# Kernel tuning notes

Hardware: AMD Instinct MI355X
Metric: run time of the kernel (lower is better)

Reference implementation:

```python
import jax, jax.numpy as jnp
import numpy as np

D_MODEL = 1024
NUM_HEADS = 16
HEAD_DIM = D_MODEL // NUM_HEADS


def setup_inputs() -> dict:
    key = jax.random.key(0)
    ks = jax.random.split(key, 11)
    S, B, D = 2048, 2, D_MODEL
    scale = 1.0 / np.sqrt(D)
    inp = {
        'query': jax.random.normal(ks[0], (S, B, D), dtype=jnp.float32),
        'key': jax.random.normal(ks[1], (S, B, D), dtype=jnp.float32),
        'value': jax.random.normal(ks[2], (S, B, D), dtype=jnp.float32),
        'Wq': jax.random.normal(ks[3], (D, D), dtype=jnp.float32) * scale,
        'bq': jnp.zeros((D,), dtype=jnp.float32),
        'Wk': jax.random.normal(ks[4], (D, D), dtype=jnp.float32) * scale,
        'bk': jnp.zeros((D,), dtype=jnp.float32),
        'Wv': jax.random.normal(ks[5], (D, D), dtype=jnp.float32) * scale,
        'bv': jnp.zeros((D,), dtype=jnp.float32),
        'Wo': jax.random.normal(ks[6], (D, D), dtype=jnp.float32) * scale,
        'bo': jnp.zeros((D,), dtype=jnp.float32),
    }
    return inp


def reference(query, key, value, Wq, bq, Wk, bk, Wv, bv, Wo, bo):
    # query/key/value: [S, B, D] (seq-first, as in the torch module)
    S, B, D = query.shape
    H, Hd = NUM_HEADS, HEAD_DIM
    # Linear: x @ W.T + b (torch convention), then split heads -> [B, H, S, Hd]
    def proj_heads(x, W, b):
        y = jnp.einsum('sbd,ed->sbe', x, W) + b  # [S, B, D]
        return y.reshape(x.shape[0], B, H, Hd).transpose(1, 2, 0, 3)
    q = proj_heads(query, Wq, bq)   # [B, H, S, Hd]
    k = proj_heads(key, Wk, bk)     # [B, H, Sk, Hd]
    v = proj_heads(value, Wv, bv)   # [B, H, Sk, Hd]
    scores = jnp.einsum('bhsd,bhtd->bhst', q, k) / jnp.sqrt(jnp.asarray(Hd, q.dtype))
    probs = jax.nn.softmax(scores, axis=-1)  # dropout p=0.0 -> identity
    attn = jnp.einsum('bhst,bhtd->bhsd', probs, v)  # [B, H, S, Hd]
    attn = attn.transpose(2, 0, 1, 3).reshape(S, B, D)  # [S, B, D]
    out = jnp.einsum('sbd,ed->sbe', attn, Wo) + bo
    return out
```

## Files before the change

kernel.cpp:

```cpp
#include <hip/hip_runtime.h>
#include <stdint.h>

#define S_LEN 2048
#define BATCH 2
#define DM    1024
#define NH    16
#define HD    64
#define MROWS 4096

typedef float f32x4 __attribute__((ext_vector_type(4)));
typedef short bfrag __attribute__((ext_vector_type(8)));
typedef unsigned short u16x4_t __attribute__((ext_vector_type(4)));
typedef unsigned short u16x8_t __attribute__((ext_vector_type(8)));
typedef int i32x4_t __attribute__((ext_vector_type(4)));

#define EXP2F(x) __builtin_amdgcn_exp2f(x)

__device__ inline f32x4 mfma16(bfrag a, bfrag b, f32x4 c) {
    return __builtin_amdgcn_mfma_f32_16x16x32_bf16(a, b, c, 0, 0, 0);
}

__device__ inline unsigned short bf16_rn(float x) {
    unsigned u = __builtin_bit_cast(unsigned, x);
    return (unsigned short)((u + 0x7fffu + ((u >> 16) & 1u)) >> 16);
}

__device__ inline void split_bf16(float x, unsigned short &h, unsigned short &l) {
    unsigned u = __builtin_bit_cast(unsigned, x);
    h = (unsigned short)(u >> 16);
    float hf = __builtin_bit_cast(float, u & 0xffff0000u);
    float r = x - hf;
    l = (unsigned short)(__builtin_bit_cast(unsigned, r) >> 16);
}

__device__ inline unsigned pack_rhu(float a, float b) {
    unsigned ua = __builtin_bit_cast(unsigned, a) + 0x8000u;
    unsigned ub = __builtin_bit_cast(unsigned, b) + 0x8000u;
    return (ua >> 16) | (ub & 0xffff0000u);
}

typedef __attribute__((address_space(1))) const unsigned int as1_u32;
typedef __attribute__((address_space(3))) unsigned int as3_u32;
__device__ inline void async16(void* lds, const void* g) {
    __builtin_amdgcn_global_load_lds((as1_u32*)g, (as3_u32*)lds, 16, 0, 0);
}

__global__ __launch_bounds__(256)
void cvt_kernel(const float* __restrict__ Wq, const float* __restrict__ Wk,
                const float* __restrict__ Wv, const float* __restrict__ Wo,
                const float* __restrict__ Qin, const float* __restrict__ Kin,
                const float* __restrict__ Vin,
                unsigned short* __restrict__ Wqb, unsigned short* __restrict__ Wkb,
                unsigned short* __restrict__ Wvb,
                unsigned short* __restrict__ Woh, unsigned short* __restrict__ Wol,
                unsigned short* __restrict__ Qa,  unsigned short* __restrict__ Ka,
                unsigned short* __restrict__ Va)
{
    const int z = blockIdx.z;
    size_t idx = ((size_t)blockIdx.x * 256 + threadIdx.x) * 8;
    const size_t limit = (z < 4) ? (size_t)DM * DM : (size_t)MROWS * DM;
    if (idx >= limit) return;
    const float* src = (z == 0) ? Wq : (z == 1) ? Wk : (z == 2) ? Wv :
                       (z == 3) ? Wo : (z == 4) ? Qin : (z == 5) ? Kin : Vin;
    float4 f0 = *(const float4*)&src[idx];
    float4 f1 = *(const float4*)&src[idx + 4];
    if (z != 3) {
        unsigned short* dst = (z == 0) ? Wqb : (z == 1) ? Wkb : (z == 2) ? Wvb :
                              (z == 4) ? Qa  : (z == 5) ? Ka  : Va;
        u16x8_t v = { bf16_rn(f0.x), bf16_rn(f0.y), bf16_rn(f0.z), bf16_rn(f0.w),
                      bf16_rn(f1.x), bf16_rn(f1.y), bf16_rn(f1.z), bf16_rn(f1.w) };
        *(u16x8_t*)&dst[idx] = v;
    } else {
        unsigned short h0,h1,h2,h3,h4,h5,h6,h7, l0,l1,l2,l3,l4,l5,l6,l7;
        split_bf16(f0.x,h0,l0); split_bf16(f0.y,h1,l1);
        split_bf16(f0.z,h2,l2); split_bf16(f0.w,h3,l3);
        split_bf16(f1.x,h4,l4); split_bf16(f1.y,h5,l5);
        split_bf16(f1.z,h6,l6); split_bf16(f1.w,h7,l7);
        u16x8_t vh = {h0,h1,h2,h3,h4,h5,h6,h7};
        u16x8_t vl = {l0,l1,l2,l3,l4,l5,l6,l7};
        *(u16x8_t*)&Woh[idx] = vh;
        *(u16x8_t*)&Wol[idx] = vl;
    }
}

__global__ __launch_bounds__(256)
void qkv_gemm(const unsigned short* __restrict__ Qa,
              const unsigned short* __restrict__ Ka,
              const unsigned short* __restrict__ Va,
              const unsigned short* __restrict__ Wqb,
              const unsigned short* __restrict__ Wkb,
              const unsigned short* __restrict__ Wvb,
              const float* __restrict__ bq, const float* __restrict__ bk,
              const float* __restrict__ bv,
              unsigned short* __restrict__ Qb, unsigned short* __restrict__ Kb,
              unsigned short* __restrict__ Vt)
{
    __shared__ unsigned short sA[128*32];
    __shared__ unsigned short sB[128*32];

    const int tid = threadIdx.x, lane = tid & 63, w4 = tid >> 6;
    const int m16 = lane & 15, q4 = lane >> 4;
    const int wr = w4 >> 1, wc = w4 & 1;
    const int z = blockIdx.z;

    int id = blockIdx.x + 8 * blockIdx.y;
    int j  = id >> 3;
    const int m0 = ((id & 7) * 4 + (j & 3)) * 128;
    const int n0 = (j >> 2) * 128;

    const unsigned short* A = (z == 0) ? Qa : (z == 1) ? Ka : Va;
    const unsigned short* W = (z == 0) ? Wqb : (z == 1) ? Wkb : Wvb;
    const float* bias = (z == 0) ? bq : (z == 1) ? bk : bv;
    unsigned short* outp = (z == 0) ? Qb : (z == 1) ? Kb : Vt;

    const int G1 = tid + 256;
    const int r0 = tid >> 2, g0 = (tid & 3) ^ ((r0 ^ (r0 >> 2)) & 3);
    const int r1 = G1  >> 2, g1 = (G1  & 3) ^ ((r1 ^ (r1 >> 2)) & 3);
    const char* gA0 = (const char*)A + (size_t)(m0 + r0) * 2048 + g0 * 16;
    const char* gA1 = (const char*)A + (size_t)(m0 + r1) * 2048 + g1 * 16;
    const char* gB0 = (const char*)W + (size_t)(n0 + r0) * 2048 + g0 * 16;
    const char* gB1 = (const char*)W + (size_t)(n0 + r1) * 2048 + g1 * 16;
    char* ldsA0 = (char*)sA + w4 * 1024;
    char* ldsA1 = (char*)sA + 4096 + w4 * 1024;
    char* ldsB0 = (char*)sB + w4 * 1024;
    char* ldsB1 = (char*)sB + 4096 + w4 * 1024;

    int offA[4], offB[4];
    #pragma unroll
    for (int rt = 0; rt < 4; rt++) {
        int r = wr * 64 + rt * 16 + m16;
        offA[rt] = r * 32 + ((q4 ^ ((r ^ (r >> 2)) & 3)) << 3);
    }
    #pragma unroll
    for (int ct = 0; ct < 4; ct++) {
        int r = wc * 64 + ct * 16 + m16;
        offB[ct] = r * 32 + ((q4 ^ ((r ^ (r >> 2)) & 3)) << 3);
    }

    f32x4 acc[4][4];
    const f32x4 zero4 = {0.f, 0.f, 0.f, 0.f};
    #pragma unroll
    for (int i = 0; i < 4; i++)
        #pragma unroll
        for (int jj = 0; jj < 4; jj++) acc[i][jj] = zero4;

    for (int k0 = 0; k0 < DM; k0 += 32) {
        async16(ldsA0, gA0);
        async16(ldsA1, gA1);
        async16(ldsB0, gB0);
        async16(ldsB1, gB1);
        gA0 += 64; gA1 += 64; gB0 += 64; gB1 += 64;
        __syncthreads();

        bfrag a[4], bb[4];
        #pragma unroll
        for (int rt = 0; rt < 4; rt++) a[rt]  = *(const bfrag*)&sA[offA[rt]];
        #pragma unroll
        for (int ct = 0; ct < 4; ct++) bb[ct] = *(const bfrag*)&sB[offB[ct]];

        #pragma unroll
        for (int rt = 0; rt < 4; rt++)
            #pragma unroll
            for (int ct = 0; ct < 4; ct++)
                acc[rt][ct] = mfma16(a[rt], bb[ct], acc[rt][ct]);
        __syncthreads();
    }

    const float SCALE = (z == 0) ? 0.18033688011112042f : 1.0f;
    #pragma unroll
    for (int rt = 0; rt < 4; rt++)
        #pragma unroll
        for (int ct = 0; ct < 4; ct++)
            #pragma unroll
            for (int reg = 0; reg < 4; reg++) {
                int r = m0 + wr * 64 + rt * 16 + q4 * 4 + reg;
                int c = n0 + wc * 64 + ct * 16 + m16;
                float v = (acc[rt][ct][reg] + bias[c]) * SCALE;
                int s = r >> 1, b = r & 1, hh = c >> 6, d = c & 63;
                unsigned short bv16 = bf16_rn(v);
                if (z == 2)
                    outp[((size_t)(b * NH + hh) * HD + d) * S_LEN + s] = bv16;
                else
                    outp[((size_t)(b * NH + hh) * S_LEN + s) * HD + d] = bv16;
            }
}

__global__ __launch_bounds__(256)
void attn_kernel(const unsigned short* __restrict__ Qb,
                 const unsigned short* __restrict__ Kb,
                 const unsigned short* __restrict__ Vt,
                 unsigned short* __restrict__ Ap)
{
    __shared__ unsigned short sK[2][64*64];
    __shared__ unsigned short sV[2][64*64];
    __shared__ unsigned int   sPT[4][32*36];

    const int tid = threadIdx.x, lane = tid & 63, w4 = tid >> 6;
    const int m16 = lane & 15, q4 = lane >> 4;

    int id = blockIdx.x;
    int xcd = id & 7, jj = id >> 3;
    const int bh = xcd * 4 + (jj >> 4);
    const int qc = jj & 15;
    const int b = bh >> 4, h = bh & 15;
    const int qw = qc * 128 + w4 * 32;

    const unsigned short* Qp = Qb + (size_t)bh * (S_LEN * HD);
    const unsigned short* Kp = Kb + (size_t)bh * (S_LEN * HD);
    const unsigned short* Vp = Vt + (size_t)bh * (S_LEN * HD);
    unsigned int* pw = sPT[w4];

    bfrag aq[2][2];
    #pragma unroll
    for (int nt = 0; nt < 2; nt++)
        #pragma unroll
        for (int kc = 0; kc < 2; kc++)
            aq[nt][kc] = *(const bfrag*)&Qp[(size_t)(qw + nt*16 + m16) * HD + kc*32 + q4*8];

    const int r0 = tid >> 3,         g0 = (tid & 7) ^ (r0 & 7);
    const int r1 = (tid + 256) >> 3, g1 = (tid & 7) ^ (r1 & 7);
    const char* gK0 = (const char*)Kp + (size_t)r0 * 128  + g0 * 16;
    const char* gK1 = (const char*)Kp + (size_t)r1 * 128  + g1 * 16;
    const char* gV0 = (const char*)Vp + (size_t)r0 * 4096 + g0 * 16;
    const char* gV1 = (const char*)Vp + (size_t)r1 * 4096 + g1 * 16;
    const int ldsw = w4 * 1024;

    const f32x4 zero4 = {0.f, 0.f, 0.f, 0.f};
    f32x4 O[2][4];
    float lp[2] = {0.f, 0.f};
    #pragma unroll
    for (int nt = 0; nt < 2; nt++)
        #pragma unroll
        for (int dt = 0; dt < 4; dt++) O[nt][dt] = zero4;

    async16((char*)sK[0] + ldsw,        gK0);
    async16((char*)sK[0] + 4096 + ldsw, gK1);
    async16((char*)sV[0] + ldsw,        gV0);
    async16((char*)sV[0] + 4096 + ldsw, gV1);

    const int NT = S_LEN / 64;
    for (int it = 0; it < NT; it++) {
        const int bi = it & 1;
        __syncthreads();
        if (it + 1 < NT) {
            size_t ko = (size_t)(it + 1) * 8192, vo = (size_t)(it + 1) * 128;
            async16((char*)sK[bi^1] + ldsw,        gK0 + ko);
            async16((char*)sK[bi^1] + 4096 + ldsw, gK1 + ko);
            async16((char*)sV[bi^1] + ldsw,        gV0 + vo);
            async16((char*)sV[bi^1] + 4096 + ldsw, gV1 + vo);
        }

        const unsigned short* kb = sK[bi];
        const unsigned short* vb = sV[bi];

        bfrag ak[4][2];
        #pragma unroll
        for (int mt = 0; mt < 4; mt++) {
            int r = mt*16 + m16, s = r & 7;
            ak[mt][0] = *(const bfrag*)&kb[r*64 + ((q4     ^ s) << 3)];
            ak[mt][1] = *(const bfrag*)&kb[r*64 + (((4+q4) ^ s) << 3)];
        }

        #pragma unroll
        for (int nt = 0; nt < 2; nt++) {
            f32x4 Sc[4];
            #pragma unroll
            for (int mt = 0; mt < 4; mt++) {
                Sc[mt] = mfma16(ak[mt][0], aq[nt][0], zero4);
                Sc[mt] = mfma16(ak[mt][1], aq[nt][1], Sc[mt]);
            }
            unsigned rowb = (unsigned)(nt*16 + m16) * 36;
            #pragma unroll
            for (int mt = 0; mt < 4; mt++) {
                float p0 = EXP2F(Sc[mt][0]), p1 = EXP2F(Sc[mt][1]);
                float p2 = EXP2F(Sc[mt][2]), p3 = EXP2F(Sc[mt][3]);
                unsigned c0 = pack_rhu(p0, p1);
                unsigned c1 = pack_rhu(p2, p3);
                float u0 = __builtin_bit_cast(float, c0 << 16);
                float u1 = __builtin_bit_cast(float, c0 & 0xffff0000u);
                float u2 = __builtin_bit_cast(float, c1 << 16);
                float u3 = __builtin_bit_cast(float, c1 & 0xffff0000u);
                lp[nt] += (u0 + u1) + (u2 + u3);
                uint2 c2 = { c0, c1 };
                *(uint2*)&pw[rowb + mt*8 + q4*2] = c2;
            }
        }

        bfrag av[4][2];
        #pragma unroll
        for (int dt = 0; dt < 4; dt++) {
            int r = dt*16 + m16, s = r & 7;
            av[dt][0] = *(const bfrag*)&vb[r*64 + ((q4     ^ s) << 3)];
            av[dt][1] = *(const bfrag*)&vb[r*64 + (((4+q4) ^ s) << 3)];
        }

        #pragma unroll
        for (int nt = 0; nt < 2; nt++) {
            bfrag bp[2];
            #pragma unroll
            for (int kc = 0; kc < 2; kc++)
                bp[kc] = __builtin_bit_cast(bfrag,
                    *(const i32x4_t*)&pw[(unsigned)(nt*16 + m16) * 36 + kc*16 + q4*4]);
            #pragma unroll
            for (int dt = 0; dt < 4; dt++) {
                O[nt][dt] = mfma16(av[dt][0], bp[0], O[nt][dt]);
                O[nt][dt] = mfma16(av[dt][1], bp[1], O[nt][dt]);
            }
        }
    }

    #pragma unroll
    for (int nt = 0; nt < 2; nt++) {
        float l = lp[nt];
        l += __shfl_xor(l, 16);
        l += __shfl_xor(l, 32);
        float inv = 1.0f / l;
        int q = qw + nt*16 + m16;
        size_t rb = ((size_t)q * BATCH + b) * DM + h * 64;
        #pragma unroll
        for (int dt = 0; dt < 4; dt++) {
            u16x4_t o = { bf16_rn(O[nt][dt][0] * inv), bf16_rn(O[nt][dt][1] * inv),
                          bf16_rn(O[nt][dt][2] * inv), bf16_rn(O[nt][dt][3] * inv) };
            *(u16x4_t*)&Ap[rb + dt*16 + q4*4] = o;
        }
    }
}

__global__ __launch_bounds__(512)
void out_gemm(const unsigned short* __restrict__ Ap,
              const unsigned short* __restrict__ Woh,
              const unsigned short* __restrict__ Wol,
              const float* __restrict__ bo, float* __restrict__ out)
{
    __shared__ unsigned short sA[128*32];
    __shared__ unsigned short sH[128*32];
    __shared__ unsigned short sL[128*32];

    const int tid = threadIdx.x, lane = tid & 63, w8 = tid >> 6;
    const int m16 = lane & 15, q4 = lane >> 4;
    const int wr = w8 >> 2, wc = w8 & 3;

    int id = blockIdx.x + 8 * blockIdx.y;
    int j  = id >> 3;
    const int m0 = ((id & 7) * 4 + (j & 3)) * 128;
    const int n0 = (j >> 2) * 128;

    const int br = tid >> 2,  bc = (tid & 3) ^ ((br ^ (br >> 2)) & 3);
    const unsigned short* gA = Ap  + (size_t)(m0 + br) * DM + bc * 8;
    const unsigned short* gH = Woh + (size_t)(n0 + br) * DM + bc * 8;
    const unsigned short* gL = Wol + (size_t)(n0 + br) * DM + bc * 8;
    unsigned short* ldsA = &sA[w8 * 512];
    unsigned short* ldsH = &sH[w8 * 512];
    unsigned short* ldsL = &sL[w8 * 512];

    int offA[4], offB[2];
    #pragma unroll
    for (int rt = 0; rt < 4; rt++) {
        int r = wr * 64 + rt * 16 + m16;
        offA[rt] = r * 32 + ((q4 ^ ((r ^ (r >> 2)) & 3)) << 3);
    }
    #pragma unroll
    for (int ct = 0; ct < 2; ct++) {
        int r = wc * 32 + ct * 16 + m16;
        offB[ct] = r * 32 + ((q4 ^ ((r ^ (r >> 2)) & 3)) << 3);
    }

    f32x4 acc[4][2];
    const f32x4 zero4 = {0.f, 0.f, 0.f, 0.f};
    #pragma unroll
    for (int i = 0; i < 4; i++)
        #pragma unroll
        for (int jj = 0; jj < 2; jj++) acc[i][jj] = zero4;

    for (int k0 = 0; k0 < DM; k0 += 32) {
        async16(ldsA, gA);
        async16(ldsH, gH);
        async16(ldsL, gL);
        gA += 32; gH += 32; gL += 32;
        __syncthreads();

        bfrag a[4], bh2[2], bl2[2];
        #pragma unroll
        for (int rt = 0; rt < 4; rt++) a[rt] = *(const bfrag*)&sA[offA[rt]];
        #pragma unroll
        for (int ct = 0; ct < 2; ct++) {
            bh2[ct] = *(const bfrag*)&sH[offB[ct]];
            bl2[ct] = *(const bfrag*)&sL[offB[ct]];
        }
        #pragma unroll
        for (int rt = 0; rt < 4; rt++)
            #pragma unroll
            for (int ct = 0; ct < 2; ct++) {
                acc[rt][ct] = mfma16(a[rt], bh2[ct], acc[rt][ct]);
                acc[rt][ct] = mfma16(a[rt], bl2[ct], acc[rt][ct]);
            }
        __syncthreads();
    }

    #pragma unroll
    for (int rt = 0; rt < 4; rt++)
        #pragma unroll
        for (int ct = 0; ct < 2; ct++)
            #pragma unroll
            for (int reg = 0; reg < 4; reg++) {
                int r = m0 + wr * 64 + rt * 16 + q4 * 4 + reg;
                int c = n0 + wc * 32 + ct * 16 + m16;
                out[(size_t)r * DM + c] = acc[rt][ct][reg] + bo[c];
            }
}

extern "C" void kernel_launch(void* const* d_in, const int* in_sizes, int n_in,
                              void* d_out, int out_size, void* d_ws, size_t ws_size,
                              hipStream_t stream)
{
    const float* query = (const float*)d_in[0];
    const float* key   = (const float*)d_in[1];
    const float* value = (const float*)d_in[2];
    const float* Wq    = (const float*)d_in[3];
    const float* bq    = (const float*)d_in[4];
    const float* Wk    = (const float*)d_in[5];
    const float* bk    = (const float*)d_in[6];
    const float* Wv    = (const float*)d_in[7];
    const float* bv    = (const float*)d_in[8];
    const float* Wo    = (const float*)d_in[9];
    const float* bo    = (const float*)d_in[10];

    char* ws = (char*)d_ws;
    const size_t MB = 1u << 20;
    unsigned short* Qb  = (unsigned short*)(ws);
    unsigned short* Kb  = (unsigned short*)(ws +  8*MB);
    unsigned short* Vt  = (unsigned short*)(ws + 16*MB);
    unsigned short* Woh = (unsigned short*)(ws + 24*MB);
    unsigned short* Wol = (unsigned short*)(ws + 26*MB);
    unsigned short* Wqb = (unsigned short*)(ws + 28*MB);
    unsigned short* Wkb = (unsigned short*)(ws + 30*MB);
    unsigned short* Wvb = (unsigned short*)(ws + 32*MB);
    unsigned short* Va  = (unsigned short*)(ws + 34*MB);
    unsigned short* Ap  = (unsigned short*)(ws + 28*MB);
    unsigned short* Qa  = (unsigned short*)d_out;
    unsigned short* Ka  = (unsigned short*)d_out + (size_t)MROWS*DM;

    cvt_kernel<<<dim3(2048, 1, 7), 256, 0, stream>>>(
        Wq, Wk, Wv, Wo, query, key, value,
        Wqb, Wkb, Wvb, Woh, Wol, Qa, Ka, Va);
    qkv_gemm<<<dim3(8, 32, 3), 256, 0, stream>>>(
        Qa, Ka, Va, Wqb, Wkb, Wvb, bq, bk, bv, Qb, Kb, Vt);
    attn_kernel<<<dim3(512), 256, 0, stream>>>(Qb, Kb, Vt, Ap);
    out_gemm<<<dim3(8, 32), 512, 0, stream>>>(Ap, Woh, Wol, bo, (float*)d_out);
}
```

Baseline: 243.8 us.

## Split attention over key halves with combine kernel and retile output GEMM

The attention kernel now splits the key/value sequence into two halves, doubling the grid to 1024 blocks. Each block writes unnormalized bf16 partial outputs and row sums, and a new combine kernel adds the halves, normalizes, and writes the head-interleaved layout. The output GEMM is retiled to 256 threads with 128x64 tiles and twice as many blocks. This aims to improve CU occupancy and load balance, at the cost of an extra kernel launch, extra memory traffic for the partials, and an extra bf16 rounding of the partial outputs. The row sum also now accumulates unrounded probabilities.

```diff
diff --git a/kernel.cpp b/kernel.cpp
--- a/kernel.cpp
+++ b/kernel.cpp
@@ -189,7 +189,8 @@
 void attn_kernel(const unsigned short* __restrict__ Qb,
                  const unsigned short* __restrict__ Kb,
                  const unsigned short* __restrict__ Vt,
-                 unsigned short* __restrict__ Ap)
+                 unsigned short* __restrict__ Op,
+                 float* __restrict__ Lp)
 {
     __shared__ unsigned short sK[2][64*64];
     __shared__ unsigned short sV[2][64*64];
@@ -199,11 +200,13 @@
     const int m16 = lane & 15, q4 = lane >> 4;
 
     int id = blockIdx.x;
-    int xcd = id & 7, jj = id >> 3;
-    const int bh = xcd * 4 + (jj >> 4);
-    const int qc = jj & 15;
-    const int b = bh >> 4, h = bh & 15;
-    const int qw = qc * 128 + w4 * 32;
+    int xcd = id & 7, j = id >> 3;
+    const int bh   = xcd * 4 + (j >> 5);
+    const int rem  = j & 31;
+    const int half = rem & 1;
+    const int qc   = rem >> 1;
+    const int qw   = qc * 128 + w4 * 32;
+    const int tbase = half * (S_LEN / 2);
 
     const unsigned short* Qp = Qb + (size_t)bh * (S_LEN * HD);
     const unsigned short* Kp = Kb + (size_t)bh * (S_LEN * HD);
@@ -219,10 +222,10 @@
 
     const int r0 = tid >> 3,         g0 = (tid & 7) ^ (r0 & 7);
     const int r1 = (tid + 256) >> 3, g1 = (tid & 7) ^ (r1 & 7);
-    const char* gK0 = (const char*)Kp + (size_t)r0 * 128  + g0 * 16;
-    const char* gK1 = (const char*)Kp + (size_t)r1 * 128  + g1 * 16;
-    const char* gV0 = (const char*)Vp + (size_t)r0 * 4096 + g0 * 16;
-    const char* gV1 = (const char*)Vp + (size_t)r1 * 4096 + g1 * 16;
+    const char* gK0 = (const char*)Kp + (size_t)(tbase + r0) * 128 + g0 * 16;
+    const char* gK1 = (const char*)Kp + (size_t)(tbase + r1) * 128 + g1 * 16;
+    const char* gV0 = (const char*)Vp + (size_t)r0 * 4096 + tbase * 2 + g0 * 16;
+    const char* gV1 = (const char*)Vp + (size_t)r1 * 4096 + tbase * 2 + g1 * 16;
     const int ldsw = w4 * 1024;
 
     const f32x4 zero4 = {0.f, 0.f, 0.f, 0.f};
@@ -238,7 +241,7 @@
     async16((char*)sV[0] + ldsw,        gV0);
     async16((char*)sV[0] + 4096 + ldsw, gV1);
 
-    const int NT = S_LEN / 64;
+    const int NT = (S_LEN / 2) / 64;
     for (int it = 0; it < NT; it++) {
         const int bi = it & 1;
         __syncthreads();
@@ -274,14 +277,8 @@
             for (int mt = 0; mt < 4; mt++) {
                 float p0 = EXP2F(Sc[mt][0]), p1 = EXP2F(Sc[mt][1]);
                 float p2 = EXP2F(Sc[mt][2]), p3 = EXP2F(Sc[mt][3]);
-                unsigned c0 = pack_rhu(p0, p1);
-                unsigned c1 = pack_rhu(p2, p3);
-                float u0 = __builtin_bit_cast(float, c0 << 16);
-                float u1 = __builtin_bit_cast(float, c0 & 0xffff0000u);
-                float u2 = __builtin_bit_cast(float, c1 << 16);
-                float u3 = __builtin_bit_cast(float, c1 & 0xffff0000u);
-                lp[nt] += (u0 + u1) + (u2 + u3);
-                uint2 c2 = { c0, c1 };
+                lp[nt] += (p0 + p1) + (p2 + p3);
+                uint2 c2 = { pack_rhu(p0, p1), pack_rhu(p2, p3) };
                 *(uint2*)&pw[rowb + mt*8 + q4*2] = c2;
             }
         }
@@ -309,49 +306,80 @@
         }
     }
 
+    const size_t OPH = (size_t)BATCH * NH * S_LEN * HD;
+    unsigned short* Ob = Op + (size_t)half * OPH;
+    float* Lb = Lp + (size_t)half * (BATCH * NH * S_LEN);
     #pragma unroll
     for (int nt = 0; nt < 2; nt++) {
         float l = lp[nt];
         l += __shfl_xor(l, 16);
         l += __shfl_xor(l, 32);
-        float inv = 1.0f / l;
         int q = qw + nt*16 + m16;
-        size_t rb = ((size_t)q * BATCH + b) * DM + h * 64;
+        if (q4 == 0) Lb[(size_t)bh * S_LEN + q] = l;
+        size_t rb = ((size_t)bh * S_LEN + q) * HD;
         #pragma unroll
         for (int dt = 0; dt < 4; dt++) {
-            u16x4_t o = { bf16_rn(O[nt][dt][0] * inv), bf16_rn(O[nt][dt][1] * inv),
-                          bf16_rn(O[nt][dt][2] * inv), bf16_rn(O[nt][dt][3] * inv) };
-            *(u16x4_t*)&Ap[rb + dt*16 + q4*4] = o;
-        }
-    }
-}
-
-__global__ __launch_bounds__(512)
+            u16x4_t o = { bf16_rn(O[nt][dt][0]), bf16_rn(O[nt][dt][1]),
+                          bf16_rn(O[nt][dt][2]), bf16_rn(O[nt][dt][3]) };
+            *(u16x4_t*)&Ob[rb + dt*16 + q4*4] = o;
+        }
+    }
+}
+
+__global__ __launch_bounds__(256)
+void cmb_kernel(const unsigned short* __restrict__ Op,
+                const float* __restrict__ Lp,
+                unsigned short* __restrict__ Ap)
+{
+    const size_t OPH = (size_t)BATCH * NH * S_LEN * HD;
+    int idx = blockIdx.x * 256 + threadIdx.x;
+    int rho = idx >> 3, dg = idx & 7;
+    size_t e = (size_t)rho * HD + dg * 8;
+    float inv = 1.0f / (Lp[rho] + Lp[BATCH*NH*S_LEN + rho]);
+    u16x8_t a = *(const u16x8_t*)&Op[e];
+    u16x8_t b2 = *(const u16x8_t*)&Op[OPH + e];
+    u16x8_t r;
+    #pragma unroll
+    for (int i = 0; i < 8; i++) {
+        float fa = __builtin_bit_cast(float, (unsigned)(unsigned short)a[i]  << 16);
+        float fb = __builtin_bit_cast(float, (unsigned)(unsigned short)b2[i] << 16);
+        r[i] = bf16_rn((fa + fb) * inv);
+    }
+    int bh = rho >> 11, q = rho & 2047;
+    int b = bh >> 4, h = bh & 15;
+    *(u16x8_t*)&Ap[((size_t)(q * 2 + b)) * DM + h * 64 + dg * 8] = r;
+}
+
+__global__ __launch_bounds__(256)
 void out_gemm(const unsigned short* __restrict__ Ap,
               const unsigned short* __restrict__ Woh,
               const unsigned short* __restrict__ Wol,
               const float* __restrict__ bo, float* __restrict__ out)
 {
     __shared__ unsigned short sA[128*32];
-    __shared__ unsigned short sH[128*32];
-    __shared__ unsigned short sL[128*32];
-
-    const int tid = threadIdx.x, lane = tid & 63, w8 = tid >> 6;
+    __shared__ unsigned short sH[64*32];
+    __shared__ unsigned short sL[64*32];
+
+    const int tid = threadIdx.x, lane = tid & 63, w4 = tid >> 6;
     const int m16 = lane & 15, q4 = lane >> 4;
-    const int wr = w8 >> 2, wc = w8 & 3;
-
-    int id = blockIdx.x + 8 * blockIdx.y;
+    const int wr = w4 >> 1, wc = w4 & 1;
+
+    int id = blockIdx.x + 16 * blockIdx.y;
     int j  = id >> 3;
     const int m0 = ((id & 7) * 4 + (j & 3)) * 128;
-    const int n0 = (j >> 2) * 128;
-
-    const int br = tid >> 2,  bc = (tid & 3) ^ ((br ^ (br >> 2)) & 3);
-    const unsigned short* gA = Ap  + (size_t)(m0 + br) * DM + bc * 8;
-    const unsigned short* gH = Woh + (size_t)(n0 + br) * DM + bc * 8;
-    const unsigned short* gL = Wol + (size_t)(n0 + br) * DM + bc * 8;
-    unsigned short* ldsA = &sA[w8 * 512];
-    unsigned short* ldsH = &sH[w8 * 512];
-    unsigned short* ldsL = &sL[w8 * 512];
+    const int n0 = (j >> 2) * 64;
+
+    const int G1 = tid + 256;
+    const int r0 = tid >> 2, g0 = (tid & 3) ^ ((r0 ^ (r0 >> 2)) & 3);
+    const int r1 = G1  >> 2, g1 = (G1  & 3) ^ ((r1 ^ (r1 >> 2)) & 3);
+    const char* gA0 = (const char*)Ap  + (size_t)(m0 + r0) * 2048 + g0 * 16;
+    const char* gA1 = (const char*)Ap  + (size_t)(m0 + r1) * 2048 + g1 * 16;
+    const char* gH  = (const char*)Woh + (size_t)(n0 + r0) * 2048 + g0 * 16;
+    const char* gL  = (const char*)Wol + (size_t)(n0 + r0) * 2048 + g0 * 16;
+    char* ldsA0 = (char*)sA + w4 * 1024;
+    char* ldsA1 = (char*)sA + 4096 + w4 * 1024;
+    char* ldsH  = (char*)sH + w4 * 1024;
+    char* ldsL  = (char*)sL + w4 * 1024;
 
     int offA[4], offB[2];
     #pragma unroll
@@ -373,10 +401,11 @@
         for (int jj = 0; jj < 2; jj++) acc[i][jj] = zero4;
 
     for (int k0 = 0; k0 < DM; k0 += 32) {
-        async16(ldsA, gA);
-        async16(ldsH, gH);
-        async16(ldsL, gL);
-        gA += 32; gH += 32; gL += 32;
+        async16(ldsA0, gA0);
+        async16(ldsA1, gA1);
+        async16(ldsH,  gH);
+        async16(ldsL,  gL);
+        gA0 += 64; gA1 += 64; gH += 64; gL += 64;
         __syncthreads();
 
         bfrag a[4], bh2[2], bl2[2];
@@ -436,7 +465,9 @@
     unsigned short* Wkb = (unsigned short*)(ws + 30*MB);
     unsigned short* Wvb = (unsigned short*)(ws + 32*MB);
     unsigned short* Va  = (unsigned short*)(ws + 34*MB);
-    unsigned short* Ap  = (unsigned short*)(ws + 28*MB);
+    float*          Lp  = (float*)         (ws + 28*MB);
+    unsigned short* Apl = (unsigned short*)(ws + 34*MB);
+    unsigned short* Opart = (unsigned short*)d_out;
     unsigned short* Qa  = (unsigned short*)d_out;
     unsigned short* Ka  = (unsigned short*)d_out + (size_t)MROWS*DM;
 
@@ -445,6 +476,7 @@
         Wqb, Wkb, Wvb, Woh, Wol, Qa, Ka, Va);
     qkv_gemm<<<dim3(8, 32, 3), 256, 0, stream>>>(
         Qa, Ka, Va, Wqb, Wkb, Wvb, bq, bk, bv, Qb, Kb, Vt);
-    attn_kernel<<<dim3(512), 256, 0, stream>>>(Qb, Kb, Vt, Ap);
-    out_gemm<<<dim3(8, 32), 512, 0, stream>>>(Ap, Woh, Wol, bo, (float*)d_out);
-}
+    attn_kernel<<<dim3(1024), 256, 0, stream>>>(Qb, Kb, Vt, Opart, Lp);
+    cmb_kernel<<<dim3(2048), 256, 0, stream>>>(Opart, Lp, Apl);
+    out_gemm<<<dim3(16, 32), 256, 0, stream>>>(Apl, Woh, Wol, bo, (float*)d_out);
+}
```

After: 238.8 us. 1.02x faster.
